# Performance work log

Hardware: AMD Instinct MI355X
Metric: run time of the kernel (lower is better)

Reference implementation:

```python
import jax, jax.numpy as jnp
import numpy as np

B, N, D, E, R = 4, 4096, 64, 131072, 64

def setup_inputs() -> dict:
    key = jax.random.key(0)
    k1, k2, k3, k4 = jax.random.split(key, 4)
    z = jax.random.normal(k1, (B, N, D), dtype=jnp.float32)
    pairs = jax.random.randint(k2, (E, 2), 0, N, dtype=jnp.int64)
    # Linear params (PyTorch convention: y = x @ W.T + b), init scale ~ 1/sqrt(fan_in)
    W1 = jax.random.normal(k3, (R, 4 * D), dtype=jnp.float32) / np.sqrt(4 * D)
    b1 = jnp.zeros((R,), dtype=jnp.float32)
    W2 = jax.random.normal(k4, (R, R), dtype=jnp.float32) / np.sqrt(R)
    b2 = jnp.zeros((R,), dtype=jnp.float32)
    return {"z": z, "pairs": pairs, "W1": W1, "b1": b1, "W2": W2, "b2": b2}

def reference(z, pairs, W1, b1, W2, b2):
    # gather endpoint embeddings: [B, E, D]
    zi = z[:, pairs[:, 0], :]
    zj = z[:, pairs[:, 1], :]
    # pair feature [B, E, 4D]: concat(zi, zj, zi-zj, zi*zj)
    pair = jnp.concatenate([zi, zj, zi - zj, zi * zj], axis=-1)
    # 2-layer MLP (dropout is identity at inference)
    h = jnp.einsum('bef,rf->ber', pair, W1) + b1
    h = jax.nn.relu(h)
    h = jnp.einsum('ber,sr->bes', h, W2) + b2
    return h
```

## Files before the change

kernel.cpp:

```cpp
#include <hip/hip_runtime.h>
#include <hip/hip_bf16.h>
#include <stdint.h>


typedef __attribute__((ext_vector_type(8))) __bf16 bf16x8;
typedef __attribute__((ext_vector_type(4))) __bf16 bf16x4;
typedef __attribute__((ext_vector_type(4))) float  f32x4;

#define E_TOT 131072
#define N_TOK 4096
#define ROWS_PER_BLOCK 512
#define NSUB 4
#define Z_ELEMS (4 * N_TOK * 64)

__global__ __launch_bounds__(256) void zcast_kernel(const float* __restrict__ z,
                                                    __bf16* __restrict__ zb)
{
    const int t = blockIdx.x * 256 + threadIdx.x;
    const float4 a = ((const float4*)z)[2 * t];
    const float4 b = ((const float4*)z)[2 * t + 1];
    bf16x8 r;
    r[0] = (__bf16)a.x; r[1] = (__bf16)a.y; r[2] = (__bf16)a.z; r[3] = (__bf16)a.w;
    r[4] = (__bf16)b.x; r[5] = (__bf16)b.y; r[6] = (__bf16)b.z; r[7] = (__bf16)b.w;
    ((bf16x8*)zb)[t] = r;
}

__device__ __forceinline__ f32x4 mfma16(bf16x8 a, bf16x8 b, f32x4 c) {
    return __builtin_amdgcn_mfma_f32_16x16x32_bf16(a, b, c, 0, 0, 0);
}

__device__ __forceinline__ bf16x8 pk8(float4 a, float4 b) {
    bf16x8 r;
    r[0] = (__bf16)a.x; r[1] = (__bf16)a.y; r[2] = (__bf16)a.z; r[3] = (__bf16)a.w;
    r[4] = (__bf16)b.x; r[5] = (__bf16)b.y; r[6] = (__bf16)b.z; r[7] = (__bf16)b.w;
    return r;
}
__device__ __forceinline__ float4 f4add(float4 a, float4 b){ return make_float4(a.x+b.x, a.y+b.y, a.z+b.z, a.w+b.w); }
__device__ __forceinline__ float4 f4sub(float4 a, float4 b){ return make_float4(a.x-b.x, a.y-b.y, a.z-b.z, a.w-b.w); }

__device__ __forceinline__ bf16x8 bmul(bf16x8 a, bf16x8 b) {
    bf16x8 r;
#pragma unroll
    for (int t = 0; t < 8; ++t)
        r[t] = (__bf16)((float)a[t] * (float)b[t]);
    return r;
}

__global__ __launch_bounds__(512, 6) void PairRelationEncoder_62775241998442_kernel(
    const __bf16* __restrict__ zw, const int* __restrict__ pairs,
    const float* __restrict__ W1, const float* __restrict__ b1,
    const float* __restrict__ W2, const float* __restrict__ b2,
    float* __restrict__ out)
{
    const int tid  = threadIdx.x;
    const int wave = tid >> 6;
    const int lane = tid & 63;
    const int x = lane & 15;
    const int g = lane >> 4;

    const int bid = (int)(blockIdx.x & 7) * 128 + ((int)blockIdx.x >> 3);
    const int m0 = bid * ROWS_PER_BLOCK;
    const int b  = m0 >> 17;
    const int e0 = m0 & (E_TOT - 1);
    const __bf16* zb = zw + ((size_t)b * N_TOK * 64);

    int2 ijv[NSUB];
#pragma unroll
    for (int st = 0; st < NSUB; ++st)
        ijv[st] = *(const int2*)(pairs + 2 * (size_t)(e0 + (st * 8 + wave) * 16 + x));

    __shared__ __bf16 w1s[64 * 192];
    __shared__ __bf16 w2s[64 * 64];
    __shared__ __bf16 h1s[8][1024];
    __shared__ float  b1s[64];
    __shared__ float  b2s[64];
    __bf16* h1w = h1s[wave];

    {
        const int part = tid >> 7;
        const int scol = tid & 63;
        const int c8b  = ((tid >> 6) & 1) * 4;
        const int cswz = (scol & 7) << 4;
        if (part < 3) {
            const float* wr = W1 + (size_t)scol * 256;
            char* dst = (char*)w1s + scol * 384;
#pragma unroll
            for (int c = 0; c < 4; ++c) {
                const int c8 = c8b + c;
                float4 p0, p1;
                if (part == 0) {
                    float4 a0 = *(const float4*)(wr + c8*8);
                    float4 a1 = *(const float4*)(wr + c8*8 + 4);
                    float4 c0 = *(const float4*)(wr + 128 + c8*8);
                    float4 c1 = *(const float4*)(wr + 128 + c8*8 + 4);
                    p0 = f4add(a0, c0); p1 = f4add(a1, c1);
                } else if (part == 1) {
                    float4 a0 = *(const float4*)(wr + 64 + c8*8);
                    float4 a1 = *(const float4*)(wr + 64 + c8*8 + 4);
                    float4 c0 = *(const float4*)(wr + 128 + c8*8);
                    float4 c1 = *(const float4*)(wr + 128 + c8*8 + 4);
                    p0 = f4sub(a0, c0); p1 = f4sub(a1, c1);
                } else {
                    p0 = *(const float4*)(wr + 192 + c8*8);
                    p1 = *(const float4*)(wr + 192 + c8*8 + 4);
                }
                *(bf16x8*)(dst + ((part * 128 + c8 * 16) ^ cswz)) = pk8(p0, p1);
            }
        } else {
            const float* wr = W2 + (size_t)scol * 64;
            char* dst = (char*)w2s + scol * 128;
#pragma unroll
            for (int c = 0; c < 4; ++c) {
                const int c8 = c8b + c;
                float4 p0 = *(const float4*)(wr + c8*8);
                float4 p1 = *(const float4*)(wr + c8*8 + 4);
                *(bf16x8*)(dst + ((c8 * 16) ^ cswz)) = pk8(p0, p1);
            }
        }
        if (tid < 16)            ((float4*)b1s)[tid]      = ((const float4*)b1)[tid];
        else if (tid < 32)       ((float4*)b2s)[tid - 16] = ((const float4*)b2)[tid - 16];
    }

    __syncthreads();

#pragma unroll
    for (int st = 0; st < NSUB; ++st) {
        const __bf16* zri = zb + (size_t)ijv[st].x * 64;
        const __bf16* zrj = zb + (size_t)ijv[st].y * 64;
        bf16x8 a0 = *(const bf16x8*)(zri + g * 8);
        bf16x8 a1 = *(const bf16x8*)(zri + 32 + g * 8);
        bf16x8 a2 = *(const bf16x8*)(zrj + g * 8);
        bf16x8 a3 = *(const bf16x8*)(zrj + 32 + g * 8);
        bf16x8 a4 = bmul(a0, a2);
        bf16x8 a5 = bmul(a1, a3);

        f32x4 acc[4];
#pragma unroll
        for (int ct = 0; ct < 4; ++ct)
            acc[ct] = *(const f32x4*)(b1s + ct * 16 + g * 4);

#pragma unroll
        for (int h = 0; h < 2; ++h) {
#pragma unroll
            for (int ct = 0; ct < 4; ++ct) {
                const int colr = ct * 16 + x;
                const int cswz = (colr & 7) << 4;
                const char* wb = (const char*)w1s + colr * 384;
                const int kb = h * 64 + g * 16;
                bf16x8 azi = *(const bf16x8*)(wb + ((kb      ) ^ cswz));
                bf16x8 azj = *(const bf16x8*)(wb + ((kb + 128) ^ cswz));
                bf16x8 apr = *(const bf16x8*)(wb + ((kb + 256) ^ cswz));
                acc[ct] = mfma16(azi, (h == 0) ? a0 : a1, acc[ct]);
                acc[ct] = mfma16(azj, (h == 0) ? a2 : a3, acc[ct]);
                acc[ct] = mfma16(apr, (h == 0) ? a4 : a5, acc[ct]);
            }
        }

#pragma unroll
        for (int ct = 0; ct < 4; ++ct) {
            bf16x4 p;
#pragma unroll
            for (int q = 0; q < 4; ++q)
                p[q] = (__bf16)fmaxf(acc[ct][q], 0.f);
            const int wo = (x * 128 + ct * 32 + g * 8) ^ ((x & 7) << 4);
            *(bf16x4*)((char*)h1w + wo) = p;
        }

        f32x4 o[4];
#pragma unroll
        for (int ct = 0; ct < 4; ++ct)
            o[ct] = *(const f32x4*)(b2s + ct * 16 + g * 4);

#pragma unroll
        for (int kk = 0; kk < 2; ++kk) {
            const int aoff = (x * 128 + kk * 64 + g * 16) ^ ((x & 7) << 4);
            const bf16x8 h1f = *(const bf16x8*)((const char*)h1w + aoff);
#pragma unroll
            for (int ct = 0; ct < 4; ++ct) {
                const int cols = ct * 16 + x;
                const bf16x8 w2f = *(const bf16x8*)((const char*)w2s + cols * 128
                                                    + ((kk * 64 + g * 16) ^ ((cols & 7) << 4)));
                o[ct] = mfma16(w2f, h1f, o[ct]);
            }
        }

        float* orow = out + ((size_t)(m0 + (st * 8 + wave) * 16 + x)) * 64;
#pragma unroll
        for (int ct = 0; ct < 4; ++ct)
            *(f32x4*)(orow + ct * 16 + g * 4) = o[ct];
    }
}

extern "C" void kernel_launch(void* const* d_in, const int* in_sizes, int n_in,
                              void* d_out, int out_size, void* d_ws, size_t ws_size,
                              hipStream_t stream) {
    const float* z     = (const float*)d_in[0];
    const int*   pairs = (const int*)  d_in[1];
    const float* W1    = (const float*)d_in[2];
    const float* b1    = (const float*)d_in[3];
    const float* W2    = (const float*)d_in[4];
    const float* b2    = (const float*)d_in[5];
    float* out = (float*)d_out;
    __bf16* zw = (__bf16*)d_ws;

    zcast_kernel<<<Z_ELEMS / (256 * 8), 256, 0, stream>>>(z, zw);

    const int total_rows = 4 * E_TOT;
    dim3 grid(total_rows / ROWS_PER_BLOCK);
    PairRelationEncoder_62775241998442_kernel<<<grid, 512, 0, stream>>>(
        zw, pairs, W1, b1, W2, b2, out);
}
```

Baseline: 53.72 us.

## Lower occupancy hint, remap weight staging threads, and load z halves lazily

The launch-bounds occupancy hint drops from 6 to 4 blocks, which gives the compiler more registers per thread. Weight-staging threads are reassigned so that each group of 64 threads handles one part, and the bias loads become scalar loads spread over 128 threads. The gathered z fragments are now loaded per half inside the h loop instead of all up front, which shortens register live ranges but may expose gather latency closer to the MFMAs. The swizzle term is hoisted out of the loop.

New measurement: 53.21 us. Within noise of the previous version (-1.0%).

```diff
diff --git a/kernel.cpp b/kernel.cpp
--- a/kernel.cpp
+++ b/kernel.cpp
@@ -46,7 +46,7 @@
     return r;
 }
 
-__global__ __launch_bounds__(512, 6) void PairRelationEncoder_62775241998442_kernel(
+__global__ __launch_bounds__(512, 4) void PairRelationEncoder_62775241998442_kernel(
     const __bf16* __restrict__ zw, const int* __restrict__ pairs,
     const float* __restrict__ W1, const float* __restrict__ b1,
     const float* __restrict__ W2, const float* __restrict__ b2,
@@ -77,9 +77,9 @@
     __bf16* h1w = h1s[wave];
 
     {
-        const int part = tid >> 7;
+        const int part = (tid >> 6) & 3;
         const int scol = tid & 63;
-        const int c8b  = ((tid >> 6) & 1) * 4;
+        const int c8b  = (tid >> 8) * 4;
         const int cswz = (scol & 7) << 4;
         if (part < 3) {
             const float* wr = W1 + (size_t)scol * 256;
@@ -117,22 +117,18 @@
                 *(bf16x8*)(dst + ((c8 * 16) ^ cswz)) = pk8(p0, p1);
             }
         }
-        if (tid < 16)            ((float4*)b1s)[tid]      = ((const float4*)b1)[tid];
-        else if (tid < 32)       ((float4*)b2s)[tid - 16] = ((const float4*)b2)[tid - 16];
+        if (tid < 64)            b1s[tid] = b1[tid];
+        else if (tid < 128)      b2s[tid - 64] = b2[tid - 64];
     }
 
     __syncthreads();
+
+    const int sw = (x & 7) << 4;
 
 #pragma unroll
     for (int st = 0; st < NSUB; ++st) {
         const __bf16* zri = zb + (size_t)ijv[st].x * 64;
         const __bf16* zrj = zb + (size_t)ijv[st].y * 64;
-        bf16x8 a0 = *(const bf16x8*)(zri + g * 8);
-        bf16x8 a1 = *(const bf16x8*)(zri + 32 + g * 8);
-        bf16x8 a2 = *(const bf16x8*)(zrj + g * 8);
-        bf16x8 a3 = *(const bf16x8*)(zrj + 32 + g * 8);
-        bf16x8 a4 = bmul(a0, a2);
-        bf16x8 a5 = bmul(a1, a3);
 
         f32x4 acc[4];
 #pragma unroll
@@ -141,18 +137,21 @@
 
 #pragma unroll
         for (int h = 0; h < 2; ++h) {
+            bf16x8 azf = *(const bf16x8*)(zri + h * 32 + g * 8);
+            bf16x8 bzf = *(const bf16x8*)(zrj + h * 32 + g * 8);
+            bf16x8 pzf = bmul(azf, bzf);
+            const int kb = h * 64 + g * 16;
 #pragma unroll
             for (int ct = 0; ct < 4; ++ct) {
                 const int colr = ct * 16 + x;
                 const int cswz = (colr & 7) << 4;
                 const char* wb = (const char*)w1s + colr * 384;
-                const int kb = h * 64 + g * 16;
-                bf16x8 azi = *(const bf16x8*)(wb + ((kb      ) ^ cswz));
-                bf16x8 azj = *(const bf16x8*)(wb + ((kb + 128) ^ cswz));
-                bf16x8 apr = *(const bf16x8*)(wb + ((kb + 256) ^ cswz));
-                acc[ct] = mfma16(azi, (h == 0) ? a0 : a1, acc[ct]);
-                acc[ct] = mfma16(azj, (h == 0) ? a2 : a3, acc[ct]);
-                acc[ct] = mfma16(apr, (h == 0) ? a4 : a5, acc[ct]);
+                bf16x8 wzi = *(const bf16x8*)(wb + ((kb      ) ^ cswz));
+                bf16x8 wzj = *(const bf16x8*)(wb + ((kb + 128) ^ cswz));
+                bf16x8 wpr = *(const bf16x8*)(wb + ((kb + 256) ^ cswz));
+                acc[ct] = mfma16(wzi, azf, acc[ct]);
+                acc[ct] = mfma16(wzj, bzf, acc[ct]);
+                acc[ct] = mfma16(wpr, pzf, acc[ct]);
             }
         }
 
@@ -162,7 +161,7 @@
 #pragma unroll
             for (int q = 0; q < 4; ++q)
                 p[q] = (__bf16)fmaxf(acc[ct][q], 0.f);
-            const int wo = (x * 128 + ct * 32 + g * 8) ^ ((x & 7) << 4);
+            const int wo = (x * 128 + ct * 32 + g * 8) ^ sw;
             *(bf16x4*)((char*)h1w + wo) = p;
         }
 
@@ -173,7 +172,7 @@
 
 #pragma unroll
         for (int kk = 0; kk < 2; ++kk) {
-            const int aoff = (x * 128 + kk * 64 + g * 16) ^ ((x & 7) << 4);
+            const int aoff = (x * 128 + kk * 64 + g * 16) ^ sw;
             const bf16x8 h1f = *(const bf16x8*)((const char*)h1w + aoff);
 #pragma unroll
             for (int ct = 0; ct < 4; ++ct) {
```
